# Optimization experiments

Measured on AMD Instinct MI355X. Metric: run time of the kernel, lower is better.

The kernel has to match this reference:

```python
import jax, jax.numpy as jnp
import numpy as np

PAD_TOKEN = 0.0
REPLACEMENT_PROB = 0.1


def setup_inputs() -> dict:
    key = jax.random.key(0)
    # item-ID-like values in [0, 100000); zeros act as pad tokens
    x = jax.random.randint(key, (16384, 2048), 0, 100000).astype(jnp.float32)
    return {"x": x}


def reference(x):
    """Stochastic Swap Noise: replace ~p of non-pad positions with values
    sampled without replacement from the non-pad values of the tensor.

    Jit-friendly equivalent of torch's
      bernoulli -> masked_select compaction -> randperm -> scatter
    chain: a single argsort on random keys (pads keyed to +2.0) both
    compacts the non-pad values to the front AND shuffles them; a cumsum
    over the replacement mask assigns each replaced position its donor.
    """
    key = jax.random.key(42)
    k_bern, k_shuf = jax.random.split(key)

    nonpad = x != PAD_TOKEN                                        # [B,S] bool
    repl = (jax.random.uniform(k_bern, x.shape) < REPLACEMENT_PROB) & nonpad

    flat_x = x.reshape(-1)                                          # [N]
    flat_nonpad = nonpad.reshape(-1)
    flat_repl = repl.reshape(-1)

    # compaction + shuffle in one sort: non-pad elems get uniform [0,1) keys,
    # pads get 2.0 so they sink to the end.
    r = jnp.where(flat_nonpad, jax.random.uniform(k_shuf, flat_x.shape), 2.0)
    order = jnp.argsort(r)
    donors = flat_x[order]                                          # shuffled non-pad values first

    # k-th replaced position (in flat order) takes donors[k]
    rank = jnp.cumsum(flat_repl) - 1                                # -1 where not replaced (masked out below)
    out = jnp.where(flat_repl, donors[rank], flat_x)
    return out.reshape(x.shape)
```

## Files before the change

### kernel.cpp

```cpp
#include <hip/hip_runtime.h>
#include <stdint.h>

static __host__ __device__ inline uint32_t rotl32(uint32_t x, int r) {
#if defined(__HIP_DEVICE_COMPILE__)
  return __builtin_amdgcn_alignbit(x, x, (uint32_t)(32 - r));
#else
  return (x << r) | (x >> (32 - r));
#endif
}

static __host__ __device__ inline void tf2x32(uint32_t k0, uint32_t k1,
                                              uint32_t x0, uint32_t x1,
                                              uint32_t& o0, uint32_t& o1) {
  uint32_t k2 = k0 ^ k1 ^ 0x1BD11BDAu;
#define TFR(a) { x0 += x1; x1 = rotl32(x1, a); x1 ^= x0; }
  x0 += k0; x1 += k1;
  TFR(13) TFR(15) TFR(26) TFR(6)
  x0 += k1; x1 += k2 + 1u;
  TFR(17) TFR(29) TFR(16) TFR(24)
  x0 += k2; x1 += k0 + 2u;
  TFR(13) TFR(15) TFR(26) TFR(6)
  x0 += k0; x1 += k1 + 3u;
  TFR(17) TFR(29) TFR(16) TFR(24)
  x0 += k1; x1 += k2 + 4u;
  TFR(13) TFR(15) TFR(26) TFR(6)
  x0 += k2; x1 += k0 + 5u;
#undef TFR
  o0 = x0; o1 = x1;
}

static __device__ inline uint32_t fold_bits(uint32_t k0, uint32_t k1, uint32_t ctr) {
  uint32_t a, b;
  tf2x32(k0, k1, 0u, ctr, a, b);
  return a ^ b;
}

#define CUT2      917504u
#define NCOARSE   56u
#define CSTRIDE   69632u
#define WPC       17u
#define NFINE     1792u
#define STRIDE    2432u
#define BSCAP     2432u
#define ELEMS_G   8192
#define GPOOL     1216u
#define WIN       4096
#define CAPDUMP   3932160u
#define MASKI     0x07FFFFFFu
#define BERN_THR  838861u



template<bool BOUNDS>
__global__ __launch_bounds__(256) void k_bern(const float* __restrict__ x,
                                              uint64_t* __restrict__ mask,
                                              uint32_t* __restrict__ rsums,
                                              uint32_t bk0, uint32_t bk1, int n) {
  __shared__ uint32_t wcnt[4];
  int tid = threadIdx.x, lane = tid & 63, wid = tid >> 6;
  int base = blockIdx.x * ELEMS_G;
  uint32_t cnt = 0;
  unsigned long long bball[4];
  for (int it = 0; it < ELEMS_G / 1024; it++) {
    int e0 = base + it * 1024 + wid * 256 + lane * 4;
    float4 xv;
    if (!BOUNDS || e0 + 3 < n) {
      xv = *reinterpret_cast<const float4*>(x + e0);
    } else {
      xv.x = (e0 + 0 < n) ? x[e0 + 0] : 0.0f;
      xv.y = (e0 + 1 < n) ? x[e0 + 1] : 0.0f;
      xv.z = (e0 + 2 < n) ? x[e0 + 2] : 0.0f;
      xv.w = (e0 + 3 < n) ? x[e0 + 3] : 0.0f;
    }
#define BERNE(e, comp)                                                    \
    {                                                                     \
      uint32_t ii = (uint32_t)(e0 + e);                                   \
      uint32_t bb = fold_bits(bk0, bk1, ii);                              \
      bool rr = (comp != 0.0f) && ((bb >> 9) < BERN_THR);                 \
      bball[e] = __ballot(rr);                                            \
    }
    BERNE(0, xv.x) BERNE(1, xv.y) BERNE(2, xv.z) BERNE(3, xv.w)
#undef BERNE
    cnt += (uint32_t)(__popcll(bball[0]) + __popcll(bball[1]) +
                      __popcll(bball[2]) + __popcll(bball[3]));
    if (lane == 0) {
      uint32_t ci = (uint32_t)blockIdx.x * 32u + (uint32_t)it * 4u + (uint32_t)wid;
      if (!BOUNDS) {
        mask[ci * 4 + 0] = bball[0]; mask[ci * 4 + 1] = bball[1];
        mask[ci * 4 + 2] = bball[2]; mask[ci * 4 + 3] = bball[3];
      } else {
        for (int e = 0; e < 4; e++)
          if ((int)(ci * 256u + (uint32_t)e * 64u) < n) mask[ci * 4 + e] = bball[e];
      }
    }
  }
  if (lane == 0) wcnt[wid] = cnt;
  __syncthreads();
  if (tid == 0) rsums[blockIdx.x] = wcnt[0] + wcnt[1] + wcnt[2] + wcnt[3];
}

template<bool BOUNDS>
__global__ __launch_bounds__(256) void k_cand(const float* __restrict__ x,
                                              uint32_t* __restrict__ dumpCursor,
                                              uint2* __restrict__ dump,
                                              uint32_t sk0, uint32_t sk1, int n) {
  __shared__ uint2 pool[GPOOL];
  __shared__ uint32_t lpoolCnt, lgbase;
  int tid = threadIdx.x, lane = tid & 63, wid = tid >> 6;
  int base = blockIdx.x * ELEMS_G;
  if (tid == 0) lpoolCnt = 0;
  __syncthreads();
  uint64_t lt = (1ull << lane) - 1ull;
  for (int it = 0; it < ELEMS_G / 1024; it++) {
    int e0 = base + it * 1024 + wid * 256 + lane * 4;
    float4 xv;
    if (!BOUNDS || e0 + 3 < n) {
      xv = *reinterpret_cast<const float4*>(x + e0);
    } else {
      xv.x = (e0 + 0 < n) ? x[e0 + 0] : 0.0f;
      xv.y = (e0 + 1 < n) ? x[e0 + 1] : 0.0f;
      xv.z = (e0 + 2 < n) ? x[e0 + 2] : 0.0f;
      xv.w = (e0 + 3 < n) ? x[e0 + 3] : 0.0f;
    }
#define CANDE(e, comp)                                                    \
    {                                                                     \
      uint32_t ii = (uint32_t)(e0 + e);                                   \
      uint32_t mm = fold_bits(sk0, sk1, ii) >> 9;                         \
      bool cand = (comp != 0.0f) && (mm < CUT2);                          \
      unsigned long long cb = __ballot(cand);                             \
      uint32_t pb = 0;                                                    \
      if (lane == 0 && cb) pb = atomicAdd(&lpoolCnt, (uint32_t)__popcll(cb)); \
      pb = __builtin_amdgcn_readfirstlane(pb);                            \
      if (cand) {                                                         \
        uint32_t slot = pb + (uint32_t)__popcll(cb & lt);                 \
        if (slot < GPOOL) {                                               \
          uint32_t v = (uint32_t)comp;                                    \
          pool[slot] = make_uint2((mm << 12) | (v >> 5),                  \
                                  ((v & 31u) << 27) | ii);                \
        }                                                                 \
      }                                                                   \
    }
    CANDE(0, xv.x) CANDE(1, xv.y) CANDE(2, xv.z) CANDE(3, xv.w)
#undef CANDE
  }
  __syncthreads();
  if (tid == 0) {
    uint32_t pc = lpoolCnt; if (pc > GPOOL) pc = GPOOL;
    lgbase = atomicAdd((unsigned int*)dumpCursor, pc);
  }
  __syncthreads();
  uint32_t pc = lpoolCnt; if (pc > GPOOL) pc = GPOOL;
  uint32_t gb = lgbase;
  for (uint32_t j = tid; j < pc; j += 256) {
    uint32_t d = gb + j;
    if (d < CAPDUMP) dump[d] = pool[j];
  }
}

__global__ void k_scan2(uint32_t* __restrict__ data0, int n0,
                        uint32_t* __restrict__ data1, int n1) {
  __shared__ uint32_t wsum[4];
  uint32_t* data = (blockIdx.x == 0) ? data0 : data1;
  int n = (blockIdx.x == 0) ? n0 : n1;
  int tid = threadIdx.x, lane = tid & 63, wid = tid >> 6;
  uint32_t running = 0;
  for (int base = 0; base < n; base += 256) {
    int i = base + tid;
    uint32_t v = (i < n) ? data[i] : 0u;
    uint32_t incl = v;
    for (int d = 1; d < 64; d <<= 1) {
      uint32_t t = __shfl_up(incl, (unsigned)d, 64);
      if (lane >= d) incl += t;
    }
    if (lane == 63) wsum[wid] = incl;
    __syncthreads();
    uint32_t woff = 0, tot = 0;
    for (int w = 0; w < 4; w++) { uint32_t s = wsum[w]; if (w < wid) woff += s; tot += s; }
    if (i < n) data[i] = running + woff + (incl - v);
    running += tot;
    __syncthreads();
  }
  if (tid == 0) data[n] = running;
}

__global__ __launch_bounds__(256) void k_regA(const uint2* __restrict__ dump,
                                              const uint32_t* __restrict__ dumpCursor,
                                              uint32_t* __restrict__ coarseCursor,
                                              uint2* __restrict__ coarse) {
  __shared__ uint2 pool2[WIN];
  __shared__ uint32_t lh[4][64];
  __shared__ uint32_t hbase[64], lgb[64], lcur[64];
  int tid = threadIdx.x, lane = tid & 63, wid = tid >> 6;
  uint32_t total = dumpCursor[0]; if (total > CAPDUMP) total = CAPDUMP;
  uint32_t wbase = blockIdx.x * (uint32_t)WIN;
  if (wbase >= total) return;
  uint32_t valid = total - wbase; if (valid > WIN) valid = WIN;
  lh[wid][lane] = 0;
  __syncthreads();
  uint2 e[WIN / 256];
#pragma unroll
  for (int q = 0; q < WIN / 256; q++) {
    uint32_t j = (uint32_t)q * 256u + (uint32_t)tid;
    e[q] = (j < valid) ? dump[wbase + j] : make_uint2(0u, 0u);
    if (j < valid) atomicAdd(&lh[wid][e[q].x >> 26], 1u);
  }
  __syncthreads();
  if (tid < 64) {
    uint32_t h = lh[0][tid] + lh[1][tid] + lh[2][tid] + lh[3][tid];
    lgb[tid] = (h && tid < NCOARSE) ? atomicAdd((unsigned int*)&coarseCursor[tid], h) : 0u;
    lcur[tid] = h;
  }
  __syncthreads();
  if (wid == 0) {
    uint32_t v = lcur[lane];
    uint32_t incl = v;
    for (int d = 1; d < 64; d <<= 1) {
      uint32_t t = __shfl_up(incl, (unsigned)d, 64);
      if (lane >= d) incl += t;
    }
    hbase[lane] = incl - v;
    lcur[lane] = incl - v;
  }
  __syncthreads();
#pragma unroll
  for (int q = 0; q < WIN / 256; q++) {
    uint32_t j = (uint32_t)q * 256u + (uint32_t)tid;
    if (j < valid) {
      uint32_t c = e[q].x >> 26;
      uint32_t lpos = atomicAdd(&lcur[c], 1u);
      pool2[lpos] = e[q];
    }
  }
  __syncthreads();
  for (uint32_t j = tid; j < valid; j += 256) {
    uint2 p = pool2[j];
    uint32_t c = p.x >> 26;
    uint32_t dst = lgb[c] + (j - hbase[c]);
    if (dst < CSTRIDE) coarse[(size_t)c * CSTRIDE + dst] = p;
  }
}

__global__ __launch_bounds__(256) void k_regB(const uint2* __restrict__ coarse,
                                              const uint32_t* __restrict__ coarseCursor,
                                              uint32_t* __restrict__ fineCursor,
                                              uint2* __restrict__ fine) {
  __shared__ uint2 pool2[WIN];
  __shared__ uint32_t lh[4][32];
  __shared__ uint32_t hbase[32], lgb[32], lcur[32];
  int tid = threadIdx.x, lane = tid & 63, wid = tid >> 6;
  uint32_t c = blockIdx.x / WPC, w = blockIdx.x % WPC;
  uint32_t ccnt = coarseCursor[c]; if (ccnt > CSTRIDE) ccnt = CSTRIDE;
  uint32_t wbase = w * (uint32_t)WIN;
  if (wbase >= ccnt) return;
  uint32_t valid = ccnt - wbase; if (valid > WIN) valid = WIN;
  const uint2* src = coarse + (size_t)c * CSTRIDE + wbase;
  if (tid < 128) lh[tid >> 5][tid & 31] = 0;
  __syncthreads();
  uint2 e[WIN / 256];
#pragma unroll
  for (int q = 0; q < WIN / 256; q++) {
    uint32_t j = (uint32_t)q * 256u + (uint32_t)tid;
    e[q] = (j < valid) ? src[j] : make_uint2(0u, 0u);
    if (j < valid) atomicAdd(&lh[wid][(e[q].x >> 21) & 31u], 1u);
  }
  __syncthreads();
  if (tid < 32) {
    uint32_t h = lh[0][tid] + lh[1][tid] + lh[2][tid] + lh[3][tid];
    lgb[tid] = h ? atomicAdd((unsigned int*)&fineCursor[c * 32u + tid], h) : 0u;
    lcur[tid] = h;
  }
  __syncthreads();
  if (wid == 0) {
    uint32_t v = (lane < 32) ? lcur[lane] : 0u;
    uint32_t incl = v;
    for (int d = 1; d < 32; d <<= 1) {
      uint32_t t = __shfl_up(incl, (unsigned)d, 64);
      if (lane >= d) incl += t;
    }
    if (lane < 32) { hbase[lane] = incl - v; lcur[lane] = incl - v; }
  }
  __syncthreads();
#pragma unroll
  for (int q = 0; q < WIN / 256; q++) {
    uint32_t j = (uint32_t)q * 256u + (uint32_t)tid;
    if (j < valid) {
      uint32_t f = (e[q].x >> 21) & 31u;
      uint32_t lpos = atomicAdd(&lcur[f], 1u);
      pool2[lpos] = e[q];
    }
  }
  __syncthreads();
  for (uint32_t j = tid; j < valid; j += 256) {
    uint2 p = pool2[j];
    uint32_t f = (p.x >> 21) & 31u;
    uint32_t dst = lgb[f] + (j - hbase[f]);
    if (dst < STRIDE) fine[(size_t)(c * 32u + f) * STRIDE + dst] = p;
  }
}

__global__ __launch_bounds__(256) void k_binsort(const uint2* __restrict__ pairs,
                                                 const uint32_t* __restrict__ binPrefix,
                                                 float* __restrict__ donors) {
  __shared__ uint2    lbuf[BSCAP];
  __shared__ uint32_t hist[512];
  __shared__ uint32_t wsums[4];
  int tid = threadIdx.x, lane = tid & 63, wid = tid >> 6;
  uint32_t bin = blockIdx.x;
  uint32_t gbase = binPrefix[bin];
  uint32_t cnt = binPrefix[bin + 1] - gbase;
  if (cnt > STRIDE) cnt = STRIDE;
  if (cnt > BSCAP) cnt = BSCAP;
  const uint2* src = pairs + (size_t)bin * STRIDE;

  for (int c = tid; c < 512; c += 256) hist[c] = 0;
  __syncthreads();
  for (uint32_t j = tid; j < cnt; j += 256)
    atomicAdd(&hist[(src[j].x >> 12) & 511u], 1u);
  __syncthreads();
  uint32_t h0 = hist[2 * tid], h1 = hist[2 * tid + 1];
  uint32_t tsum = h0 + h1;
  uint32_t incl = tsum;
  for (int d = 1; d < 64; d <<= 1) {
    uint32_t t = __shfl_up(incl, (unsigned)d, 64);
    if (lane >= d) incl += t;
  }
  if (lane == 63) wsums[wid] = incl;
  __syncthreads();
  if (wid == 0) {
    uint32_t v = (lane < 4) ? wsums[lane] : 0u;
    uint32_t in2 = v;
    for (int d = 1; d < 4; d <<= 1) {
      uint32_t t = __shfl_up(in2, (unsigned)d, 64);
      if (lane >= d) in2 += t;
    }
    if (lane < 4) wsums[lane] = in2 - v;
  }
  __syncthreads();
  uint32_t texcl = wsums[wid] + (incl - tsum);
  uint32_t e0 = texcl, e1 = e0 + h0;
  __syncthreads();
  hist[2 * tid] = e0; hist[2 * tid + 1] = e1;
  __syncthreads();
  for (uint32_t j = tid; j < cnt; j += 256) {
    uint2 p = src[j];
    uint32_t c = (p.x >> 12) & 511u;
    uint32_t lpos = atomicAdd(&hist[c], 1u);
    lbuf[lpos] = p;
  }
  __syncthreads();
  for (int c = tid; c < 512; c += 256) {
    uint32_t lo = (c == 0) ? 0u : hist[c - 1];
    uint32_t hi = hist[c];
    for (uint32_t u = lo + 1; u < hi; u++) {
      uint2 v = lbuf[u];
      uint32_t w = u;
      while (w > lo && (lbuf[w - 1].y & MASKI) > (v.y & MASKI)) {
        lbuf[w] = lbuf[w - 1];
        w--;
      }
      lbuf[w] = v;
    }
  }
  __syncthreads();
  for (uint32_t j = tid; j < cnt; j += 256) {
    uint2 p = lbuf[j];
    uint32_t v = ((p.x & 0xFFFu) << 5) | (p.y >> 27);
    donors[gbase + j] = (float)v;
  }
}

template<bool BOUNDS>
__global__ __launch_bounds__(256) void k_final(const float* __restrict__ x,
                                               const uint64_t* __restrict__ mask,
                                               const uint32_t* __restrict__ rsums,
                                               const float* __restrict__ donors,
                                               float* __restrict__ out, int n) {
  __shared__ uint64_t lw[ELEMS_G / 64];
  __shared__ uint32_t ctot[32], cpre[32];
  int tid = threadIdx.x, lane = tid & 63, wid = tid >> 6;
  int base = blockIdx.x * ELEMS_G;
  int wordBase = blockIdx.x * (ELEMS_G / 64);
  if (tid < ELEMS_G / 64) {
    uint64_t w = 0ull;
    int wI = wordBase + tid;
    if (!BOUNDS || (((wI >> 2) * 256) + ((wI & 3) * 64) < n)) w = mask[wI];
    lw[tid] = w;
  }
  __syncthreads();
  if (tid < 32) {
    ctot[tid] = (uint32_t)(__popcll(lw[4 * tid]) + __popcll(lw[4 * tid + 1]) +
                           __popcll(lw[4 * tid + 2]) + __popcll(lw[4 * tid + 3]));
  }
  __syncthreads();
  if (tid == 0) {
    uint32_t run = 0;
    for (int c = 0; c < 32; c++) { cpre[c] = run; run += ctot[c]; }
  }
  __syncthreads();
  uint32_t rbase = rsums[blockIdx.x];
  uint64_t lt = (1ull << lane) - 1ull;
  for (int it = 0; it < ELEMS_G / 1024; it++) {
    int c = it * 4 + wid;
    uint64_t b0 = lw[c * 4 + 0], b1 = lw[c * 4 + 1],
             b2 = lw[c * 4 + 2], b3 = lw[c * 4 + 3];
    uint32_t running = rbase + cpre[c];
    int e0 = base + it * 1024 + wid * 256 + lane * 4;
    uint32_t below = (uint32_t)(__popcll(b0 & lt) + __popcll(b1 & lt) +
                                __popcll(b2 & lt) + __popcll(b3 & lt));
    uint32_t r0 = (uint32_t)((b0 >> lane) & 1ull), r1 = (uint32_t)((b1 >> lane) & 1ull);
    uint32_t r2 = (uint32_t)((b2 >> lane) & 1ull), r3 = (uint32_t)((b3 >> lane) & 1ull);
    uint32_t rk = running + below;
    float4 xv;
    if (!BOUNDS || e0 + 3 < n) {
      xv = *reinterpret_cast<const float4*>(x + e0);
    } else {
      xv.x = (e0 + 0 < n) ? x[e0 + 0] : 0.0f;
      xv.y = (e0 + 1 < n) ? x[e0 + 1] : 0.0f;
      xv.z = (e0 + 2 < n) ? x[e0 + 2] : 0.0f;
      xv.w = (e0 + 3 < n) ? x[e0 + 3] : 0.0f;
    }
    float4 ov;
    ov.x = r0 ? donors[rk] : xv.x;               rk += r0;
    ov.y = r1 ? donors[rk] : xv.y;               rk += r1;
    ov.z = r2 ? donors[rk] : xv.z;               rk += r2;
    ov.w = r3 ? donors[rk] : xv.w;
    if (!BOUNDS || e0 + 3 < n) {
      *reinterpret_cast<float4*>(out + e0) = ov;
    } else {
      if (e0 + 0 < n) out[e0 + 0] = ov.x;
      if (e0 + 1 < n) out[e0 + 1] = ov.y;
      if (e0 + 2 < n) out[e0 + 2] = ov.z;
      if (e0 + 3 < n) out[e0 + 3] = ov.w;
    }
  }
}

extern "C" void kernel_launch(void* const* d_in, const int* in_sizes, int n_in,
                              void* d_out, int out_size, void* d_ws, size_t ws_size,
                              hipStream_t stream) {
  const float* x = (const float*)d_in[0];
  float* out = (float*)d_out;
  int n = in_sizes[0];
  (void)n_in; (void)out_size; (void)ws_size;

  uint32_t bk0, bk1, sk0, sk1;
  tf2x32(0u, 42u, 0u, 0u, bk0, bk1);
  tf2x32(0u, 42u, 0u, 1u, sk0, sk1);

  int nBlkG = (n + ELEMS_G - 1) / ELEMS_G;
  bool exact = ((n % ELEMS_G) == 0);

  size_t off = 0;
  auto alloc = [&](size_t bytes) -> void* {
    void* p = (uint8_t*)d_ws + off;
    off += (bytes + 255) & ~(size_t)255;
    return p;
  };
  uint32_t* dumpCursor   = (uint32_t*)alloc(4);
  uint32_t* coarseCursor = (uint32_t*)alloc((size_t)64 * 4);
  uint32_t* fineCursor   = (uint32_t*)alloc((size_t)(NFINE + 1) * 4);
  size_t zeroBytes = off;
  uint32_t* rsums = (uint32_t*)alloc((size_t)(nBlkG + 1) * 4);
  uint64_t* mask  = (uint64_t*)alloc((size_t)((n + 63) / 64 + 4) * 8);
  uint2* bufA = (uint2*)alloc((size_t)NFINE * STRIDE * 8);
  uint2* bufB = (uint2*)alloc((size_t)NCOARSE * CSTRIDE * 8);
  uint2* dump = bufA;
  uint2* coarse = bufB;
  uint2* fine = bufA;
  float* donors = (float*)bufB;

  hipMemsetAsync(d_ws, 0, zeroBytes, stream);

  if (exact) {
    k_bern<false><<<nBlkG, 256, 0, stream>>>(x, mask, rsums, bk0, bk1, n);
    k_cand<false><<<nBlkG, 256, 0, stream>>>(x, dumpCursor, dump, sk0, sk1, n);
  } else {
    k_bern<true><<<nBlkG, 256, 0, stream>>>(x, mask, rsums, bk0, bk1, n);
    k_cand<true><<<nBlkG, 256, 0, stream>>>(x, dumpCursor, dump, sk0, sk1, n);
  }
  int nWinA = (int)(CAPDUMP / WIN);
  k_regA<<<nWinA, 256, 0, stream>>>(dump, dumpCursor, coarseCursor, coarse);
  k_regB<<<(int)(NCOARSE * WPC), 256, 0, stream>>>(coarse, coarseCursor, fineCursor, fine);
  k_scan2<<<2, 256, 0, stream>>>(rsums, nBlkG, fineCursor, (int)NFINE);
  k_binsort<<<(int)NFINE, 256, 0, stream>>>(fine, fineCursor, donors);
  if (exact)
    k_final<false><<<nBlkG, 256, 0, stream>>>(x, mask, rsums, donors, out, n);
  else
    k_final<true><<<nBlkG, 256, 0, stream>>>(x, mask, rsums, donors, out, n);
}
```

Before: 330.0 us.

## Fuse bernoulli, candidate and coarse-bucket scatter into one generation kernel

Merges the bernoulli-mask kernel, the candidate-selection kernel and the first radix regrouping pass (k_regA) into a single kernel k_gen. Each block now reads x once, computes both RNG streams, and buckets its candidates by coarse key in shared memory before scattering them straight into the coarse buffer. This drops a second full read of the input, the intermediate dump buffer round trip, and two kernel launches. In exchange the kernel holds more shared memory and registers, and the coarse scatter is done in smaller per-block chunks, so global writes are less coalesced and there are more atomics on the coarse cursors.

```diff
diff --git a/kernel.cpp b/kernel.cpp
--- a/kernel.cpp
+++ b/kernel.cpp
@@ -45,21 +45,31 @@
 #define ELEMS_G   8192
 #define GPOOL     1216u
 #define WIN       4096
-#define CAPDUMP   3932160u
 #define MASKI     0x07FFFFFFu
 #define BERN_THR  838861u
 
 
 
 template<bool BOUNDS>
-__global__ __launch_bounds__(256) void k_bern(const float* __restrict__ x,
-                                              uint64_t* __restrict__ mask,
-                                              uint32_t* __restrict__ rsums,
-                                              uint32_t bk0, uint32_t bk1, int n) {
+__global__ __launch_bounds__(256) void k_gen(const float* __restrict__ x,
+                                             uint64_t* __restrict__ mask,
+                                             uint32_t* __restrict__ rsums,
+                                             uint32_t* __restrict__ coarseCursor,
+                                             uint2* __restrict__ coarse,
+                                             uint32_t bk0, uint32_t bk1,
+                                             uint32_t sk0, uint32_t sk1, int n) {
+  __shared__ uint2 pool[GPOOL];
+  __shared__ uint2 pool2[GPOOL];
+  __shared__ uint32_t lh[64], hbase[64], lgb[64], lcur[64];
   __shared__ uint32_t wcnt[4];
+  __shared__ uint32_t lpoolCnt;
   int tid = threadIdx.x, lane = tid & 63, wid = tid >> 6;
   int base = blockIdx.x * ELEMS_G;
+  if (tid == 0) lpoolCnt = 0;
+  __syncthreads();
+
   uint32_t cnt = 0;
+  uint64_t lt = (1ull << lane) - 1ull;
   unsigned long long bball[4];
   for (int it = 0; it < ELEMS_G / 1024; it++) {
     int e0 = base + it * 1024 + wid * 256 + lane * 4;
@@ -72,61 +82,15 @@
       xv.z = (e0 + 2 < n) ? x[e0 + 2] : 0.0f;
       xv.w = (e0 + 3 < n) ? x[e0 + 3] : 0.0f;
     }
-#define BERNE(e, comp)                                                    \
+#define GENE(e, comp)                                                     \
     {                                                                     \
       uint32_t ii = (uint32_t)(e0 + e);                                   \
+      bool np = (comp != 0.0f);                                           \
       uint32_t bb = fold_bits(bk0, bk1, ii);                              \
-      bool rr = (comp != 0.0f) && ((bb >> 9) < BERN_THR);                 \
+      bool rr = np && ((bb >> 9) < BERN_THR);                             \
       bball[e] = __ballot(rr);                                            \
-    }
-    BERNE(0, xv.x) BERNE(1, xv.y) BERNE(2, xv.z) BERNE(3, xv.w)
-#undef BERNE
-    cnt += (uint32_t)(__popcll(bball[0]) + __popcll(bball[1]) +
-                      __popcll(bball[2]) + __popcll(bball[3]));
-    if (lane == 0) {
-      uint32_t ci = (uint32_t)blockIdx.x * 32u + (uint32_t)it * 4u + (uint32_t)wid;
-      if (!BOUNDS) {
-        mask[ci * 4 + 0] = bball[0]; mask[ci * 4 + 1] = bball[1];
-        mask[ci * 4 + 2] = bball[2]; mask[ci * 4 + 3] = bball[3];
-      } else {
-        for (int e = 0; e < 4; e++)
-          if ((int)(ci * 256u + (uint32_t)e * 64u) < n) mask[ci * 4 + e] = bball[e];
-      }
-    }
-  }
-  if (lane == 0) wcnt[wid] = cnt;
-  __syncthreads();
-  if (tid == 0) rsums[blockIdx.x] = wcnt[0] + wcnt[1] + wcnt[2] + wcnt[3];
-}
-
-template<bool BOUNDS>
-__global__ __launch_bounds__(256) void k_cand(const float* __restrict__ x,
-                                              uint32_t* __restrict__ dumpCursor,
-                                              uint2* __restrict__ dump,
-                                              uint32_t sk0, uint32_t sk1, int n) {
-  __shared__ uint2 pool[GPOOL];
-  __shared__ uint32_t lpoolCnt, lgbase;
-  int tid = threadIdx.x, lane = tid & 63, wid = tid >> 6;
-  int base = blockIdx.x * ELEMS_G;
-  if (tid == 0) lpoolCnt = 0;
-  __syncthreads();
-  uint64_t lt = (1ull << lane) - 1ull;
-  for (int it = 0; it < ELEMS_G / 1024; it++) {
-    int e0 = base + it * 1024 + wid * 256 + lane * 4;
-    float4 xv;
-    if (!BOUNDS || e0 + 3 < n) {
-      xv = *reinterpret_cast<const float4*>(x + e0);
-    } else {
-      xv.x = (e0 + 0 < n) ? x[e0 + 0] : 0.0f;
-      xv.y = (e0 + 1 < n) ? x[e0 + 1] : 0.0f;
-      xv.z = (e0 + 2 < n) ? x[e0 + 2] : 0.0f;
-      xv.w = (e0 + 3 < n) ? x[e0 + 3] : 0.0f;
-    }
-#define CANDE(e, comp)                                                    \
-    {                                                                     \
-      uint32_t ii = (uint32_t)(e0 + e);                                   \
       uint32_t mm = fold_bits(sk0, sk1, ii) >> 9;                         \
-      bool cand = (comp != 0.0f) && (mm < CUT2);                          \
+      bool cand = np && (mm < CUT2);                                      \
       unsigned long long cb = __ballot(cand);                             \
       uint32_t pb = 0;                                                    \
       if (lane == 0 && cb) pb = atomicAdd(&lpoolCnt, (uint32_t)__popcll(cb)); \
@@ -140,20 +104,56 @@
         }                                                                 \
       }                                                                   \
     }
-    CANDE(0, xv.x) CANDE(1, xv.y) CANDE(2, xv.z) CANDE(3, xv.w)
-#undef CANDE
-  }
-  __syncthreads();
-  if (tid == 0) {
-    uint32_t pc = lpoolCnt; if (pc > GPOOL) pc = GPOOL;
-    lgbase = atomicAdd((unsigned int*)dumpCursor, pc);
-  }
-  __syncthreads();
+    GENE(0, xv.x) GENE(1, xv.y) GENE(2, xv.z) GENE(3, xv.w)
+#undef GENE
+    cnt += (uint32_t)(__popcll(bball[0]) + __popcll(bball[1]) +
+                      __popcll(bball[2]) + __popcll(bball[3]));
+    if (lane == 0) {
+      uint32_t ci = (uint32_t)blockIdx.x * 32u + (uint32_t)it * 4u + (uint32_t)wid;
+      if (!BOUNDS) {
+        mask[ci * 4 + 0] = bball[0]; mask[ci * 4 + 1] = bball[1];
+        mask[ci * 4 + 2] = bball[2]; mask[ci * 4 + 3] = bball[3];
+      } else {
+        for (int e = 0; e < 4; e++)
+          if ((int)(ci * 256u + (uint32_t)e * 64u) < n) mask[ci * 4 + e] = bball[e];
+      }
+    }
+  }
+  if (lane == 0) wcnt[wid] = cnt;
+  if (tid < 64) lh[tid] = 0;
+  __syncthreads();
+  if (tid == 0) rsums[blockIdx.x] = wcnt[0] + wcnt[1] + wcnt[2] + wcnt[3];
   uint32_t pc = lpoolCnt; if (pc > GPOOL) pc = GPOOL;
-  uint32_t gb = lgbase;
+  for (uint32_t j = tid; j < pc; j += 256) atomicAdd(&lh[pool[j].x >> 26], 1u);
+  __syncthreads();
+  if (tid < 64) {
+    uint32_t h = lh[tid];
+    lgb[tid] = (h && tid < NCOARSE) ? atomicAdd((unsigned int*)&coarseCursor[tid], h) : 0u;
+  }
+  __syncthreads();
+  if (wid == 0) {
+    uint32_t v = lh[lane];
+    uint32_t incl = v;
+    for (int d = 1; d < 64; d <<= 1) {
+      uint32_t t = __shfl_up(incl, (unsigned)d, 64);
+      if (lane >= d) incl += t;
+    }
+    hbase[lane] = incl - v;
+    lcur[lane] = incl - v;
+  }
+  __syncthreads();
   for (uint32_t j = tid; j < pc; j += 256) {
-    uint32_t d = gb + j;
-    if (d < CAPDUMP) dump[d] = pool[j];
+    uint2 p = pool[j];
+    uint32_t c = p.x >> 26;
+    uint32_t lpos = atomicAdd(&lcur[c], 1u);
+    pool2[lpos] = p;
+  }
+  __syncthreads();
+  for (uint32_t j = tid; j < pc; j += 256) {
+    uint2 p = pool2[j];
+    uint32_t c = p.x >> 26;
+    uint32_t dst = lgb[c] + (j - hbase[c]);
+    if (dst < CSTRIDE) coarse[(size_t)c * CSTRIDE + dst] = p;
   }
 }
 
@@ -181,63 +181,6 @@
     __syncthreads();
   }
   if (tid == 0) data[n] = running;
-}
-
-__global__ __launch_bounds__(256) void k_regA(const uint2* __restrict__ dump,
-                                              const uint32_t* __restrict__ dumpCursor,
-                                              uint32_t* __restrict__ coarseCursor,
-                                              uint2* __restrict__ coarse) {
-  __shared__ uint2 pool2[WIN];
-  __shared__ uint32_t lh[4][64];
-  __shared__ uint32_t hbase[64], lgb[64], lcur[64];
-  int tid = threadIdx.x, lane = tid & 63, wid = tid >> 6;
-  uint32_t total = dumpCursor[0]; if (total > CAPDUMP) total = CAPDUMP;
-  uint32_t wbase = blockIdx.x * (uint32_t)WIN;
-  if (wbase >= total) return;
-  uint32_t valid = total - wbase; if (valid > WIN) valid = WIN;
-  lh[wid][lane] = 0;
-  __syncthreads();
-  uint2 e[WIN / 256];
-#pragma unroll
-  for (int q = 0; q < WIN / 256; q++) {
-    uint32_t j = (uint32_t)q * 256u + (uint32_t)tid;
-    e[q] = (j < valid) ? dump[wbase + j] : make_uint2(0u, 0u);
-    if (j < valid) atomicAdd(&lh[wid][e[q].x >> 26], 1u);
-  }
-  __syncthreads();
-  if (tid < 64) {
-    uint32_t h = lh[0][tid] + lh[1][tid] + lh[2][tid] + lh[3][tid];
-    lgb[tid] = (h && tid < NCOARSE) ? atomicAdd((unsigned int*)&coarseCursor[tid], h) : 0u;
-    lcur[tid] = h;
-  }
-  __syncthreads();
-  if (wid == 0) {
-    uint32_t v = lcur[lane];
-    uint32_t incl = v;
-    for (int d = 1; d < 64; d <<= 1) {
-      uint32_t t = __shfl_up(incl, (unsigned)d, 64);
-      if (lane >= d) incl += t;
-    }
-    hbase[lane] = incl - v;
-    lcur[lane] = incl - v;
-  }
-  __syncthreads();
-#pragma unroll
-  for (int q = 0; q < WIN / 256; q++) {
-    uint32_t j = (uint32_t)q * 256u + (uint32_t)tid;
-    if (j < valid) {
-      uint32_t c = e[q].x >> 26;
-      uint32_t lpos = atomicAdd(&lcur[c], 1u);
-      pool2[lpos] = e[q];
-    }
-  }
-  __syncthreads();
-  for (uint32_t j = tid; j < valid; j += 256) {
-    uint2 p = pool2[j];
-    uint32_t c = p.x >> 26;
-    uint32_t dst = lgb[c] + (j - hbase[c]);
-    if (dst < CSTRIDE) coarse[(size_t)c * CSTRIDE + dst] = p;
-  }
 }
 
 __global__ __launch_bounds__(256) void k_regB(const uint2* __restrict__ coarse,
@@ -456,30 +399,23 @@
     off += (bytes + 255) & ~(size_t)255;
     return p;
   };
-  uint32_t* dumpCursor   = (uint32_t*)alloc(4);
   uint32_t* coarseCursor = (uint32_t*)alloc((size_t)64 * 4);
   uint32_t* fineCursor   = (uint32_t*)alloc((size_t)(NFINE + 1) * 4);
   size_t zeroBytes = off;
   uint32_t* rsums = (uint32_t*)alloc((size_t)(nBlkG + 1) * 4);
   uint64_t* mask  = (uint64_t*)alloc((size_t)((n + 63) / 64 + 4) * 8);
-  uint2* bufA = (uint2*)alloc((size_t)NFINE * STRIDE * 8);
-  uint2* bufB = (uint2*)alloc((size_t)NCOARSE * CSTRIDE * 8);
-  uint2* dump = bufA;
-  uint2* coarse = bufB;
-  uint2* fine = bufA;
-  float* donors = (float*)bufB;
+  uint2* fine   = (uint2*)alloc((size_t)NFINE * STRIDE * 8);
+  uint2* coarse = (uint2*)alloc((size_t)NCOARSE * CSTRIDE * 8);
+  float* donors = (float*)coarse;
 
   hipMemsetAsync(d_ws, 0, zeroBytes, stream);
 
-  if (exact) {
-    k_bern<false><<<nBlkG, 256, 0, stream>>>(x, mask, rsums, bk0, bk1, n);
-    k_cand<false><<<nBlkG, 256, 0, stream>>>(x, dumpCursor, dump, sk0, sk1, n);
-  } else {
-    k_bern<true><<<nBlkG, 256, 0, stream>>>(x, mask, rsums, bk0, bk1, n);
-    k_cand<true><<<nBlkG, 256, 0, stream>>>(x, dumpCursor, dump, sk0, sk1, n);
-  }
-  int nWinA = (int)(CAPDUMP / WIN);
-  k_regA<<<nWinA, 256, 0, stream>>>(dump, dumpCursor, coarseCursor, coarse);
+  if (exact)
+    k_gen<false><<<nBlkG, 256, 0, stream>>>(x, mask, rsums, coarseCursor, coarse,
+                                            bk0, bk1, sk0, sk1, n);
+  else
+    k_gen<true><<<nBlkG, 256, 0, stream>>>(x, mask, rsums, coarseCursor, coarse,
+                                           bk0, bk1, sk0, sk1, n);
   k_regB<<<(int)(NCOARSE * WPC), 256, 0, stream>>>(coarse, coarseCursor, fineCursor, fine);
   k_scan2<<<2, 256, 0, stream>>>(rsums, nBlkG, fineCursor, (int)NFINE);
   k_binsort<<<(int)NFINE, 256, 0, stream>>>(fine, fineCursor, donors);
```

After: 303.1 us. -8.2%, faster.
